# Optimization experiments

Hardware: AMD Instinct MI355X
Metric: run time of the kernel (lower is better)

## Reference

```python
import jax, jax.numpy as jnp
import numpy as np

TAU = 2.0          # LIF membrane time constant (spikingjelly default)
V_TH = 1.0         # v_threshold
V_RESET = 0.0      # hard reset value
ATAN_ALPHA = 2.0   # surrogate.ATan default alpha
EPS = 1e-12        # F.normalize eps

@jax.custom_vjp
def spike_fn(x):
    # Heaviside forward, ATan surrogate backward
    return (x >= 0).astype(x.dtype)

def _spike_fwd(x):
    return spike_fn(x), x

def _spike_bwd(x, g):
    sg = (ATAN_ALPHA / 2.0) / (1.0 + (jnp.pi / 2.0 * ATAN_ALPHA * x) ** 2)
    return (g * sg,)

spike_fn.defvjp(_spike_fwd, _spike_bwd)

def setup_inputs() -> dict:
    key = jax.random.key(0)
    k1, k2 = jax.random.split(key)
    T, B, F, H = 32, 512, 2048, 2048
    x_seq = jax.random.normal(k1, (T, B, F), dtype=jnp.float32)
    lim = float(np.sqrt(6.0 / (F + H)))  # xavier_uniform
    W = jax.random.uniform(k2, (H, F), dtype=jnp.float32, minval=-lim, maxval=lim)
    b = jnp.zeros((H,), dtype=jnp.float32)
    return {"x_seq": x_seq, "W": W, "b": b}

def reference(x_seq, W, b):
    # Linear: [T,B,F] @ [F,H] -> [T,B,H]
    cur = jnp.einsum('tbf,hf->tbh', x_seq, W) + b
    # F.normalize(dim=-1): L2 normalize the injected current per neuron vector
    norm = jnp.maximum(jnp.sqrt(jnp.sum(cur * cur, axis=-1, keepdims=True)), EPS)
    cur = cur / norm

    def step(v, c):
        # LIF charge: v <- v + (x - (v - v_reset)) / tau
        v = v + (c - (v - V_RESET)) / TAU
        s = spike_fn(v - V_TH)
        sd = jax.lax.stop_gradient(s)  # detach_reset=True
        v = v * (1.0 - sd) + V_RESET * sd  # hard reset
        return v, s

    v0 = jnp.zeros(cur.shape[1:], dtype=cur.dtype)  # [B,H]
    _, spk_seq = jax.lax.scan(step, v0, cur)  # spk_seq: [T,B,H]
    count = spk_seq.sum(axis=0)  # [B,H]
    return spk_seq, count
```

## Files before the change

kernel.cpp:

```cpp
#include <hip/hip_runtime.h>
#include <hip/hip_bf16.h>

#define T_SZ 32
#define B_SZ 512
#define F_SZ 2048
#define H_SZ 2048
#define M_SZ (T_SZ * B_SZ)

#define BM 256
#define BN 128
#define BK 64
#define NT (F_SZ / BK)
#define ABYTES (BM * BK)
#define BBYTES (BN * BK)
#define TILE_BYTES (ABYTES + BBYTES)

typedef int   i32x8  __attribute__((ext_vector_type(8)));
typedef float f32x16 __attribute__((ext_vector_type(16)));

__device__ __forceinline__ void gload_lds16(const void* g, void* l) {
    __builtin_amdgcn_global_load_lds(
        (const __attribute__((address_space(1))) unsigned int*)g,
        (__attribute__((address_space(3))) unsigned int*)l,
        16, 0, 0);
}

__device__ __forceinline__ float bf16_bits_to_f32(unsigned short u) {
    return __uint_as_float(((unsigned)u) << 16);
}

__device__ __forceinline__ void sbar() {
    __builtin_amdgcn_sched_barrier(0);
    __builtin_amdgcn_s_barrier();
    __builtin_amdgcn_sched_barrier(0);
}

#define MFMA_FP8(a, b, c) __builtin_amdgcn_mfma_scale_f32_32x32x64_f8f6f4( \
        (a), (b), (c), 0 , 0 , 0, 0x7f7f7f7f, 0, 0x7f7f7f7f)

__global__ __launch_bounds__(256) void cvt_fp8_kernel(const float* __restrict__ in,
                                                      unsigned int* __restrict__ out,
                                                      float scale, int n8) {
    int i = blockIdx.x * 256 + threadIdx.x;
    if (i >= n8) return;
    float4 v0 = ((const float4*)in)[2 * i];
    float4 v1 = ((const float4*)in)[2 * i + 1];
    int w0 = __builtin_amdgcn_cvt_pk_fp8_f32(v0.x * scale, v0.y * scale, 0, false);
    w0     = __builtin_amdgcn_cvt_pk_fp8_f32(v0.z * scale, v0.w * scale, w0, true);
    int w1 = __builtin_amdgcn_cvt_pk_fp8_f32(v1.x * scale, v1.y * scale, 0, false);
    w1     = __builtin_amdgcn_cvt_pk_fp8_f32(v1.z * scale, v1.w * scale, w1, true);
    ((uint2*)out)[i] = make_uint2((unsigned)w0, (unsigned)w1);
}

__global__ __launch_bounds__(256) void init_ss_kernel(float4* __restrict__ ss4) {
    ss4[blockIdx.x * 256 + threadIdx.x] = make_float4(0.f, 0.f, 0.f, 0.f);
}

__global__ __launch_bounds__(256, 2) void gemm_fp8_kernel(const unsigned char* __restrict__ A,
                                                          const unsigned char* __restrict__ Bt,
                                                          const float* __restrict__ bias,
                                                          __hip_bfloat16* __restrict__ C,
                                                          float* __restrict__ ss)
{
    __shared__ __align__(16) unsigned char smem[2 * TILE_BYTES];

    const int tid  = threadIdx.x;
    const int lane = tid & 63;
    const int wave = tid >> 6;
    const int wm   = wave >> 1;
    const int wn   = wave & 1;
    const int l31  = lane & 31;
    const int kh   = lane >> 5;

    const int flat = blockIdx.y * 16 + blockIdx.x;
    const int swz  = (flat & 7) * 128 + (flat >> 3);
    const int n0   = (swz & 15) * BN;
    const int m0   = (swz >> 4) * BM;

    const unsigned char* const Ap = A  + (size_t)m0 * F_SZ;
    const unsigned char* const Bp = Bt + (size_t)n0 * F_SZ;

    int sAg[4], sAl[4];
    #pragma unroll
    for (int j = 0; j < 4; ++j) {
        const int c = j * 256 + tid;
        const int row = c >> 2;
        const int u = (c & 3) ^ (row & 3);
        sAg[j] = row * F_SZ + u * 16;
        sAl[j] = c * 16;
    }
    int sBg[2], sBl[2];
    #pragma unroll
    for (int j = 0; j < 2; ++j) {
        const int c = j * 256 + tid;
        const int row = c >> 2;
        const int u = (c & 3) ^ (row & 3);
        sBg[j] = row * F_SZ + u * 16;
        sBl[j] = c * 16;
    }

    int aoff[4][2], boff[2][2];
    #pragma unroll
    for (int mi = 0; mi < 4; ++mi) {
        const int ra = wm * 128 + mi * 32 + l31;
        #pragma unroll
        for (int j = 0; j < 2; ++j)
            aoff[mi][j] = ra * BK + (((kh * 2 + j) ^ (ra & 3)) * 16);
    }
    #pragma unroll
    for (int ni = 0; ni < 2; ++ni) {
        const int rb = wn * 64 + ni * 32 + l31;
        #pragma unroll
        for (int j = 0; j < 2; ++j)
            boff[ni][j] = rb * BK + (((kh * 2 + j) ^ (rb & 3)) * 16);
    }

    auto stageA = [&](int p, int kt) {
        unsigned char* const d = smem + p * TILE_BYTES;
        #pragma unroll
        for (int j = 0; j < 4; ++j) gload_lds16(Ap + kt * BK + sAg[j], d + sAl[j]);
    };
    auto stageB = [&](int p, int kt) {
        unsigned char* const d = smem + p * TILE_BYTES + ABYTES;
        #pragma unroll
        for (int j = 0; j < 2; ++j) gload_lds16(Bp + kt * BK + sBg[j], d + sBl[j]);
    };

    f32x16 acc[4][2] = {};

    stageB(0, 0);
    stageA(0, 0);
    stageB(1, 1);
    asm volatile("s_waitcnt vmcnt(2)" ::: "memory");
    sbar();

    #pragma unroll 1
    for (int kt = 0; kt < NT; ++kt) {
        unsigned char* const buf = smem + (kt & 1) * TILE_BYTES;
        unsigned char* const Bs  = buf + ABYTES;

        i32x8 a01[2], a23[2], bq[2];

        #pragma unroll
        for (int ni = 0; ni < 2; ++ni) {
            ((int4*)&bq[ni])[0] = *(const int4*)(Bs + boff[ni][0]);
            ((int4*)&bq[ni])[1] = *(const int4*)(Bs + boff[ni][1]);
        }
        #pragma unroll
        for (int mi = 0; mi < 2; ++mi) {
            ((int4*)&a01[mi])[0] = *(const int4*)(buf + aoff[mi][0]);
            ((int4*)&a01[mi])[1] = *(const int4*)(buf + aoff[mi][1]);
        }
        if (kt + 1 < NT) stageA((kt + 1) & 1, kt + 1);

        __builtin_amdgcn_s_setprio(1);
        acc[0][0] = MFMA_FP8(a01[0], bq[0], acc[0][0]);
        acc[0][1] = MFMA_FP8(a01[0], bq[1], acc[0][1]);
        acc[1][0] = MFMA_FP8(a01[1], bq[0], acc[1][0]);
        acc[1][1] = MFMA_FP8(a01[1], bq[1], acc[1][1]);
        __builtin_amdgcn_s_setprio(0);
        sbar();

        #pragma unroll
        for (int mi = 0; mi < 2; ++mi) {
            ((int4*)&a23[mi])[0] = *(const int4*)(buf + aoff[2 + mi][0]);
            ((int4*)&a23[mi])[1] = *(const int4*)(buf + aoff[2 + mi][1]);
        }
        if (kt + 2 < NT) stageB(kt & 1, kt + 2);

        __builtin_amdgcn_s_setprio(1);
        acc[2][0] = MFMA_FP8(a23[0], bq[0], acc[2][0]);
        acc[2][1] = MFMA_FP8(a23[0], bq[1], acc[2][1]);
        acc[3][0] = MFMA_FP8(a23[1], bq[0], acc[3][0]);
        acc[3][1] = MFMA_FP8(a23[1], bq[1], acc[3][1]);
        __builtin_amdgcn_s_setprio(0);

        if (kt < NT - 2)       { asm volatile("s_waitcnt vmcnt(2)" ::: "memory"); }
        else if (kt == NT - 2) { asm volatile("s_waitcnt vmcnt(0)" ::: "memory"); }
        if (kt < NT - 1) sbar();
    }

    float bv[2];
    #pragma unroll
    for (int ni = 0; ni < 2; ++ni) bv[ni] = bias[n0 + wn * 64 + ni * 32 + l31];
    #pragma unroll
    for (int mi = 0; mi < 4; ++mi) {
        const int gmb = m0 + wm * 128 + mi * 32 + 4 * kh;
        #pragma unroll
        for (int r = 0; r < 16; ++r) {
            const int grow = gmb + (r & 3) + 8 * (r >> 2);
            float p = 0.f;
            #pragma unroll
            for (int ni = 0; ni < 2; ++ni) {
                const int gn = n0 + wn * 64 + ni * 32 + l31;
                const float val = acc[mi][ni][r] * (1.0f / 256.0f) + bv[ni];
                C[(size_t)grow * H_SZ + gn] = __float2bfloat16(val);
                p += val * val;
            }
            p += __shfl_xor(p, 1, 64);
            p += __shfl_xor(p, 2, 64);
            p += __shfl_xor(p, 4, 64);
            p += __shfl_xor(p, 8, 64);
            p += __shfl_xor(p, 16, 64);
            if (l31 == 0) atomicAdd(ss + grow, p);
        }
    }
}

__global__ __launch_bounds__(256) void lif_scan_kernel(const __hip_bfloat16* __restrict__ cur,
                                                       const float* __restrict__ ss,
                                                       float* __restrict__ spk,
                                                       float* __restrict__ cnt)
{
    __shared__ float s_inv[T_SZ];
    const int gid = blockIdx.x * 256 + threadIdx.x;
    const int b   = gid >> 9;
    const int h0  = (gid & 511) * 4;

    if (threadIdx.x < T_SZ)
        s_inv[threadIdx.x] = 1.0f / fmaxf(sqrtf(ss[threadIdx.x * B_SZ + b]), 1e-12f);
    __syncthreads();

    const size_t stride = (size_t)B_SZ * H_SZ;
    const size_t base   = (size_t)b * H_SZ + h0;
    const __hip_bfloat16* p = cur + base;

    ushort4 pk[3];
    pk[0] = *(const ushort4*)(p);
    pk[1] = *(const ushort4*)(p + stride);
    pk[2] = *(const ushort4*)(p + 2 * stride);

    float v[4]  = {0, 0, 0, 0};
    float cn[4] = {0, 0, 0, 0};
    #pragma unroll
    for (int t = 0; t < T_SZ; ++t) {
        const ushort4 k = pk[t % 3];
        if (t + 3 < T_SZ) pk[t % 3] = *(const ushort4*)(p + (size_t)(t + 3) * stride);
        const float inv = s_inv[t];
        float so[4];
        {
            float c;
            c = bf16_bits_to_f32(k.x) * inv; v[0] += (c - v[0]) * 0.5f;
            c = bf16_bits_to_f32(k.y) * inv; v[1] += (c - v[1]) * 0.5f;
            c = bf16_bits_to_f32(k.z) * inv; v[2] += (c - v[2]) * 0.5f;
            c = bf16_bits_to_f32(k.w) * inv; v[3] += (c - v[3]) * 0.5f;
        }
        #pragma unroll
        for (int j = 0; j < 4; ++j) {
            float s = (v[j] >= 1.0f) ? 1.0f : 0.0f;
            so[j] = s;
            cn[j] += s;
            v[j] = (s != 0.f) ? 0.f : v[j];
        }
        *(float4*)(spk + base + (size_t)t * stride) = make_float4(so[0], so[1], so[2], so[3]);
    }
    *(float4*)(cnt + base) = make_float4(cn[0], cn[1], cn[2], cn[3]);
}

extern "C" void kernel_launch(void* const* d_in, const int* in_sizes, int n_in,
                              void* d_out, int out_size, void* d_ws, size_t ws_size,
                              hipStream_t stream) {
    const float* x    = (const float*)d_in[0];
    const float* W    = (const float*)d_in[1];
    const float* bias = (const float*)d_in[2];

    float* spk = (float*)d_out;
    float* cnt = spk + (size_t)T_SZ * B_SZ * H_SZ;

    char* ws = (char*)d_ws;
    unsigned char* x8    = (unsigned char*)ws;
    unsigned char* W8    = x8 + (size_t)M_SZ * F_SZ;
    __hip_bfloat16* curb = (__hip_bfloat16*)(W8 + (size_t)H_SZ * F_SZ);
    float* ss            = (float*)((char*)curb + (size_t)M_SZ * H_SZ * 2);

    init_ss_kernel<<<M_SZ / 1024, 256, 0, stream>>>((float4*)ss);
    cvt_fp8_kernel<<<(M_SZ * F_SZ / 8) / 256, 256, 0, stream>>>(x, (unsigned int*)x8, 1.0f,   M_SZ * F_SZ / 8);
    cvt_fp8_kernel<<<(H_SZ * F_SZ / 8) / 256, 256, 0, stream>>>(W, (unsigned int*)W8, 256.0f, H_SZ * F_SZ / 8);
    gemm_fp8_kernel<<<dim3(H_SZ / BN, M_SZ / BM), 256, 0, stream>>>(x8, W8, bias, curb, ss);
    lif_scan_kernel<<<(B_SZ * H_SZ / 4) / 256, 256, 0, stream>>>(curb, ss, spk, cnt);
}
```

Baseline: 373.3 us.

## Triple-buffer LDS tiles with one barrier per k-step and a new XOR swizzle

Moves the FP8 GEMM main loop from a double buffer with split A/B staging and two barriers per iteration to a three-stage LDS ring. Tiles kt+2 are prefetched while kt is consumed, so only one barrier per k-step is needed. All A fragments are loaded up front. The LDS swizzle changes from row&3 to (row>>1)&3 to reduce bank conflicts on fragment reads. LDS use grows to 72KB per block, which may limit the two-blocks-per-CU occupancy, and more fragment registers are held live at once.

```diff
diff --git a/kernel.cpp b/kernel.cpp
--- a/kernel.cpp
+++ b/kernel.cpp
@@ -62,7 +62,7 @@
                                                           __hip_bfloat16* __restrict__ C,
                                                           float* __restrict__ ss)
 {
-    __shared__ __align__(16) unsigned char smem[2 * TILE_BYTES];
+    __shared__ __align__(16) unsigned char smem[3 * TILE_BYTES];
 
     const int tid  = threadIdx.x;
     const int lane = tid & 63;
@@ -85,7 +85,7 @@
     for (int j = 0; j < 4; ++j) {
         const int c = j * 256 + tid;
         const int row = c >> 2;
-        const int u = (c & 3) ^ (row & 3);
+        const int u = (c & 3) ^ ((row >> 1) & 3);
         sAg[j] = row * F_SZ + u * 16;
         sAl[j] = c * 16;
     }
@@ -94,7 +94,7 @@
     for (int j = 0; j < 2; ++j) {
         const int c = j * 256 + tid;
         const int row = c >> 2;
-        const int u = (c & 3) ^ (row & 3);
+        const int u = (c & 3) ^ ((row >> 1) & 3);
         sBg[j] = row * F_SZ + u * 16;
         sBl[j] = c * 16;
     }
@@ -105,14 +105,14 @@
         const int ra = wm * 128 + mi * 32 + l31;
         #pragma unroll
         for (int j = 0; j < 2; ++j)
-            aoff[mi][j] = ra * BK + (((kh * 2 + j) ^ (ra & 3)) * 16);
+            aoff[mi][j] = ra * BK + (((kh * 2 + j) ^ ((ra >> 1) & 3)) * 16);
     }
     #pragma unroll
     for (int ni = 0; ni < 2; ++ni) {
         const int rb = wn * 64 + ni * 32 + l31;
         #pragma unroll
         for (int j = 0; j < 2; ++j)
-            boff[ni][j] = rb * BK + (((kh * 2 + j) ^ (rb & 3)) * 16);
+            boff[ni][j] = rb * BK + (((kh * 2 + j) ^ ((rb >> 1) & 3)) * 16);
     }
 
     auto stageA = [&](int p, int kt) {
@@ -128,19 +128,18 @@
 
     f32x16 acc[4][2] = {};
 
-    stageB(0, 0);
-    stageA(0, 0);
-    stageB(1, 1);
-    asm volatile("s_waitcnt vmcnt(2)" ::: "memory");
+    stageA(0, 0); stageB(0, 0);
+    stageA(1, 1); stageB(1, 1);
+    asm volatile("s_waitcnt vmcnt(6)" ::: "memory");
     sbar();
 
+    int cur = 0;
     #pragma unroll 1
     for (int kt = 0; kt < NT; ++kt) {
-        unsigned char* const buf = smem + (kt & 1) * TILE_BYTES;
+        unsigned char* const buf = smem + cur * TILE_BYTES;
         unsigned char* const Bs  = buf + ABYTES;
 
         i32x8 a01[2], a23[2], bq[2];
-
         #pragma unroll
         for (int ni = 0; ni < 2; ++ni) {
             ((int4*)&bq[ni])[0] = *(const int4*)(Bs + boff[ni][0]);
@@ -150,34 +149,34 @@
         for (int mi = 0; mi < 2; ++mi) {
             ((int4*)&a01[mi])[0] = *(const int4*)(buf + aoff[mi][0]);
             ((int4*)&a01[mi])[1] = *(const int4*)(buf + aoff[mi][1]);
-        }
-        if (kt + 1 < NT) stageA((kt + 1) & 1, kt + 1);
+            ((int4*)&a23[mi])[0] = *(const int4*)(buf + aoff[2 + mi][0]);
+            ((int4*)&a23[mi])[1] = *(const int4*)(buf + aoff[2 + mi][1]);
+        }
+
+        const int nx2 = cur;
+        (void)nx2;
+        if (kt + 2 < NT) {
+            const int p2 = (cur + 2 >= 3) ? cur - 1 : cur + 2;
+            stageA(p2, kt + 2);
+            stageB(p2, kt + 2);
+        }
 
         __builtin_amdgcn_s_setprio(1);
         acc[0][0] = MFMA_FP8(a01[0], bq[0], acc[0][0]);
         acc[0][1] = MFMA_FP8(a01[0], bq[1], acc[0][1]);
         acc[1][0] = MFMA_FP8(a01[1], bq[0], acc[1][0]);
         acc[1][1] = MFMA_FP8(a01[1], bq[1], acc[1][1]);
-        __builtin_amdgcn_s_setprio(0);
-        sbar();
-
-        #pragma unroll
-        for (int mi = 0; mi < 2; ++mi) {
-            ((int4*)&a23[mi])[0] = *(const int4*)(buf + aoff[2 + mi][0]);
-            ((int4*)&a23[mi])[1] = *(const int4*)(buf + aoff[2 + mi][1]);
-        }
-        if (kt + 2 < NT) stageB(kt & 1, kt + 2);
-
-        __builtin_amdgcn_s_setprio(1);
         acc[2][0] = MFMA_FP8(a23[0], bq[0], acc[2][0]);
         acc[2][1] = MFMA_FP8(a23[0], bq[1], acc[2][1]);
         acc[3][0] = MFMA_FP8(a23[1], bq[0], acc[3][0]);
         acc[3][1] = MFMA_FP8(a23[1], bq[1], acc[3][1]);
         __builtin_amdgcn_s_setprio(0);
 
-        if (kt < NT - 2)       { asm volatile("s_waitcnt vmcnt(2)" ::: "memory"); }
+        if (kt < NT - 2)       { asm volatile("s_waitcnt vmcnt(6)" ::: "memory"); }
         else if (kt == NT - 2) { asm volatile("s_waitcnt vmcnt(0)" ::: "memory"); }
         if (kt < NT - 1) sbar();
+
+        cur = (cur + 1 >= 3) ? 0 : cur + 1;
     }
 
     float bv[2];
```

After: 364.0 us. -2.5%, faster.
